# Kernel optimization log

Measured on AMD Instinct MI355X. Metric: run time of the kernel, lower is better.

Reference implementation:

```python
import jax, jax.numpy as jnp
import numpy as np

B, S, D, H_FF, E, NH, K = 8, 1024, 128, 512, 4, 8, 2


def setup_inputs() -> dict:
    key = jax.random.key(0)
    ks = jax.random.split(key, 8)
    g = lambda k, shape, s=0.02: jax.random.normal(k, shape, dtype=jnp.float32) * s
    return {
        "x": jax.random.normal(ks[0], (B, S, D), dtype=jnp.float32),
        "Wqkv": g(ks[1], (D, 3 * D)),
        "bqkv": jnp.zeros((3 * D,), jnp.float32),
        "Wo": g(ks[2], (D, D)),
        "bo": jnp.zeros((D,), jnp.float32),
        "n1_w": jnp.ones((D,), jnp.float32),
        "n1_b": jnp.zeros((D,), jnp.float32),
        "n2_w": jnp.ones((D,), jnp.float32),
        "n2_b": jnp.zeros((D,), jnp.float32),
        "w_gate": g(ks[3], (D, E)),
        "W1": g(ks[4], (E, D, H_FF)),
        "b1": jnp.zeros((E, H_FF), jnp.float32),
        "W2": g(ks[5], (E, H_FF, D)),
        "b2": jnp.zeros((E, D), jnp.float32),
        "num_heads": NH,
        "topk": K,
    }


def _instance_norm(x, w, b, eps=1e-5):
    # InstanceNorm1d applied over the sequence axis, per (batch, channel), affine per channel
    mu = x.mean(axis=1, keepdims=True)
    var = x.var(axis=1, keepdims=True)  # biased variance, as in torch InstanceNorm
    return (x - mu) * jax.lax.rsqrt(var + eps) * w + b


def _cv_sq(v, eps=1e-10):
    return v.var(ddof=1) / (v.mean() ** 2 + eps)


def _forward(x, Wqkv, bqkv, Wo, bo, n1_w, n1_b, n2_w, n2_b, w_gate, W1, b1, W2, b2, num_heads, topk):
    B_, S_, D_ = x.shape
    hd = D_ // num_heads
    # --- MHA ---
    qkv = x @ Wqkv + bqkv  # [B,S,3D]
    q, k, v = jnp.split(qkv, 3, axis=-1)
    rs = lambda t: t.reshape(B_, S_, num_heads, hd).transpose(0, 2, 1, 3)  # [B,H,S,hd]
    q, k, v = rs(q), rs(k), rs(v)
    scores = jnp.einsum('bhqd,bhkd->bhqk', q, k) / jnp.sqrt(jnp.float32(hd))
    attn = jax.nn.softmax(scores, axis=-1)
    o = jnp.einsum('bhqk,bhkd->bhqd', attn, v).transpose(0, 2, 1, 3).reshape(B_, S_, D_)
    h = _instance_norm(o @ Wo + bo + x, n1_w, n1_b)
    # --- MoE feedforward: node-level top-k gating (eval mode: no gating noise) ---
    flat = h.reshape(-1, D_)                      # [N, D], N = B*S tokens
    logits = flat @ w_gate                        # [N, E]
    top_logits, top_idx = jax.lax.top_k(logits, topk)
    top_gates = jax.nn.softmax(top_logits, axis=-1)
    N = flat.shape[0]
    gates = jnp.zeros_like(logits).at[jnp.arange(N)[:, None], top_idx].set(top_gates)
    hid = jax.nn.relu(jnp.einsum('nd,edh->neh', flat, W1) + b1)   # [N,E,H]
    eo = jnp.einsum('neh,ehd->ned', hid, W2) + b2                 # [N,E,D]
    y = jnp.einsum('ne,ned->nd', gates, eo).reshape(B_, S_, D_)
    importance = gates.sum(axis=0)
    load = (gates > 0).astype(jnp.float32).sum(axis=0)
    moe_loss = _cv_sq(importance) + _cv_sq(load)
    out = _instance_norm(y + h, n2_w, n2_b)
    return out, moe_loss


def reference(x, Wqkv, bqkv, Wo, bo, n1_w, n1_b, n2_w, n2_b, w_gate, W1, b1, W2, b2, num_heads, topk):
    out, _moe_loss = _forward(x, Wqkv, bqkv, Wo, bo, n1_w, n1_b, n2_w, n2_b,
                              w_gate, W1, b1, W2, b2, num_heads, topk)
    return out
```

## Files before the change

kernel.cpp:

```cpp
#include <hip/hip_runtime.h>
#include <hip/hip_bf16.h>

#define B_   8
#define S_   1024
#define D_   128
#define NH_  8
#define HD_  16
#define E_   4
#define HFF_ 512
#define NTOK (B_*S_)

typedef unsigned short ushort_t;
typedef __attribute__((ext_vector_type(8))) short bf16x8;
typedef __attribute__((ext_vector_type(4))) float f32x4;
typedef __attribute__((ext_vector_type(4))) _Float16 f16x4;
typedef __attribute__((ext_vector_type(8))) _Float16 f16x8v;

static __device__ __forceinline__ ushort_t f2bf(float f) {
    union { float f; unsigned u; } v; v.f = f;
    unsigned r = v.u + 0x7FFF + ((v.u >> 16) & 1);
    return (ushort_t)(r >> 16);
}
static __device__ __forceinline__ float bf2f(ushort_t u) {
    union { unsigned u; float f; } v; v.u = ((unsigned)u) << 16;
    return v.f;
}

__global__ __launch_bounds__(256)
void prep(const float* __restrict__ x, const float* __restrict__ Wqkv,
          const float* __restrict__ Wo, const float* __restrict__ W1,
          const float* __restrict__ W2,
          ushort_t* __restrict__ xb, ushort_t* __restrict__ Wqkv_t,
          ushort_t* __restrict__ Wo_t, ushort_t* __restrict__ W1t,
          ushort_t* __restrict__ W2t)
{
    const int seg = blockIdx.y;
    const int i = blockIdx.x * 256 + threadIdx.x;
    if (seg == 0) {
        float4 v = ((const float4*)x)[i];
        ushort4 u; u.x = f2bf(v.x); u.y = f2bf(v.y); u.z = f2bf(v.z); u.w = f2bf(v.w);
        ((ushort4*)xb)[i] = u;
    } else if (seg == 1) {
        if (i < D_ * 3 * D_) {
            int r = i / (3 * D_), c = i % (3 * D_);
            Wqkv_t[c * D_ + r] = f2bf(Wqkv[i]);
        }
    } else if (seg == 2) {
        if (i < D_ * D_) {
            int r = i >> 7, c = i & 127;
            Wo_t[c * D_ + r] = f2bf(Wo[i]);
        }
    } else if (seg == 3) {
        int e = i >> 16, rem = i & 65535, r = rem >> 9, c = rem & 511;
        W1t[e * 65536 + c * 128 + r] = f2bf(W1[i]);
    } else {
        int e = i >> 16, rem = i & 65535, k2 = rem >> 7, dd = rem & 127;
        W2t[e * 65536 + dd * 512 + k2] = f2bf(W2[i]);
    }
}

__global__ __launch_bounds__(256)
void gemm_qkv(const ushort_t* __restrict__ A, const ushort_t* __restrict__ Bt,
              const float* __restrict__ bias,
              _Float16* __restrict__ pq, _Float16* __restrict__ pk,
              _Float16* __restrict__ pv)
{
    __shared__ __align__(16) ushort_t As[4][128][8];
    __shared__ __align__(16) ushort_t Bs[4][128][8];
    const int bm = blockIdx.x * 128;
    const int bn = blockIdx.y * 128;
    const int part = blockIdx.y;
    const int tid = threadIdx.x;
    const int l = tid & 63, wv = tid >> 6;
    const int lc = l & 15, lg = l >> 4;
    const int wr = wv >> 1, wc = wv & 1;
    const int K = D_;

    f32x4 acc[4][4] = {};

    const int srow = tid & 127, sch = tid >> 7;
    const ushort_t* ap = A + (size_t)(bm + srow) * K + sch * 8;
    const ushort_t* bp = Bt + (size_t)(bn + srow) * K + sch * 8;

    for (int k0 = 0; k0 < K; k0 += 32) {
        *(bf16x8*)As[sch][srow]     = *(const bf16x8*)(ap + k0);
        *(bf16x8*)As[sch + 2][srow] = *(const bf16x8*)(ap + k0 + 16);
        *(bf16x8*)Bs[sch][srow]     = *(const bf16x8*)(bp + k0);
        *(bf16x8*)Bs[sch + 2][srow] = *(const bf16x8*)(bp + k0 + 16);
        __syncthreads();
        bf16x8 af[4], bfr[4];
        #pragma unroll
        for (int f = 0; f < 4; f++) {
            af[f]  = *(const bf16x8*)As[lg][wr * 64 + f * 16 + lc];
            bfr[f] = *(const bf16x8*)Bs[lg][wc * 64 + f * 16 + lc];
        }
        #pragma unroll
        for (int fm = 0; fm < 4; fm++)
            #pragma unroll
            for (int fn = 0; fn < 4; fn++)
                acc[fm][fn] = __builtin_amdgcn_mfma_f32_16x16x32_bf16(
                    af[fm], bfr[fn], acc[fm][fn], 0, 0, 0);
        __syncthreads();
    }

    #pragma unroll
    for (int fm = 0; fm < 4; fm++) {
        #pragma unroll
        for (int fn = 0; fn < 4; fn++) {
            const int col = bn + wc * 64 + fn * 16 + lc;
            const int hh = (col >> 4) & 7, dd = col & 15;
            const int row0 = bm + wr * 64 + fm * 16 + lg * 4;
            const int b = row0 >> 10, s0 = row0 & 1023;
            const size_t bh = (size_t)(b * NH_ + hh);
            const float bcol = bias[col];
            if (part == 2) {
                f16x4 vv;
                #pragma unroll
                for (int rr = 0; rr < 4; rr++)
                    vv[rr] = (_Float16)(acc[fm][fn][rr] + bcol);
                *(f16x4*)&pv[(bh << 14) + (dd << 10) + s0] = vv;
            } else {
                const float sc = (part == 0) ? 0.36067376022224085f : 1.f;
                _Float16* dst = (part == 0) ? pq : pk;
                #pragma unroll
                for (int rr = 0; rr < 4; rr++)
                    dst[(bh * 1024 + s0 + rr) * HD_ + dd] =
                        (_Float16)((acc[fm][fn][rr] + bcol) * sc);
            }
        }
    }
}

__global__ __launch_bounds__(256)
void gemm_out(const ushort_t* __restrict__ attno, const ushort_t* __restrict__ Wo_t,
              const float* __restrict__ bo, const float* __restrict__ x,
              float* __restrict__ t, float* __restrict__ pstat)
{
    __shared__ __align__(16) ushort_t As[4][64][8];
    __shared__ __align__(16) ushort_t Bs[4][128][8];
    __shared__ float2 sred[4][128];
    const int tok0 = blockIdx.x * 64;
    const int tid = threadIdx.x;
    const int l = tid & 63, wv = tid >> 6;
    const int lc = l & 15, lg = l >> 4;

    f32x4 acc[8] = {};

    const int arow = tid & 63, akc = tid >> 6;
    const int bn = tid & 127, bj = tid >> 7;
    const ushort_t* ap = attno + (size_t)(tok0 + arow) * D_ + akc * 8;
    const ushort_t* bp = Wo_t + (size_t)bn * D_ + bj * 16;

    for (int k0 = 0; k0 < 128; k0 += 32) {
        *(bf16x8*)As[akc][arow]     = *(const bf16x8*)(ap + k0);
        *(bf16x8*)Bs[bj * 2][bn]     = *(const bf16x8*)(bp + k0);
        *(bf16x8*)Bs[bj * 2 + 1][bn] = *(const bf16x8*)(bp + k0 + 8);
        __syncthreads();
        bf16x8 af = *(const bf16x8*)As[lg][wv * 16 + lc];
        #pragma unroll
        for (int fn = 0; fn < 8; fn++) {
            bf16x8 bf = *(const bf16x8*)Bs[lg][fn * 16 + lc];
            acc[fn] = __builtin_amdgcn_mfma_f32_16x16x32_bf16(af, bf, acc[fn], 0, 0, 0);
        }
        __syncthreads();
    }

    const int bb = tok0 >> 10, c16 = (tok0 >> 6) & 15;
    #pragma unroll
    for (int fn = 0; fn < 8; fn++) {
        const int col = fn * 16 + lc;
        float s = 0.f, q = 0.f;
        #pragma unroll
        for (int rr = 0; rr < 4; rr++) {
            const int row = wv * 16 + lg * 4 + rr;
            const size_t off = (size_t)(tok0 + row) * D_ + col;
            float v = acc[fn][rr] + bo[col] + x[off];
            t[off] = v;
            s += v; q += v * v;
        }
        s += __shfl_xor(s, 16); q += __shfl_xor(q, 16);
        s += __shfl_xor(s, 32); q += __shfl_xor(q, 32);
        if (l < 16) sred[wv][col] = make_float2(s, q);
    }
    __syncthreads();
    if (tid < 128) {
        float2 a0 = sred[0][tid], a1 = sred[1][tid], a2 = sred[2][tid], a3 = sred[3][tid];
        ((float2*)pstat)[(bb * 16 + c16) * D_ + tid] =
            make_float2(a0.x + a1.x + a2.x + a3.x, a0.y + a1.y + a2.y + a3.y);
    }
}

__global__ __launch_bounds__(256)
void moe_fused(const ushort_t* __restrict__ hb, const ushort_t* __restrict__ W1t,
               const ushort_t* __restrict__ W2t, const float* __restrict__ b1,
               const float* __restrict__ b2, const float* __restrict__ gates,
               ushort_t* __restrict__ ypartb)
{
    __shared__ __align__(16) ushort_t As[16][64][8];
    __shared__ __align__(16) ushort_t HS[16][64][8];
    const int tok0 = blockIdx.x * 64, e = blockIdx.y;
    const int tid = threadIdx.x;
    const int l = tid & 63, wv = tid >> 6;
    const int lc = l & 15, lg = l >> 4;

    {
        const int row = tid & 63, part = tid >> 6;
        const ushort_t* src = hb + (size_t)(tok0 + row) * D_ + part * 32;
        #pragma unroll
        for (int j = 0; j < 4; j++)
            *(bf16x8*)As[part * 4 + j][row] = *(const bf16x8*)(src + j * 8);
    }
    __syncthreads();

    const ushort_t* W1e = W1t + (size_t)e * HFF_ * D_;
    const ushort_t* W2e = W2t + (size_t)e * D_ * HFF_;
    const int col0 = wv * 32 + lc;

    f32x4 acc2[4][2] = {};

    #pragma unroll 1
    for (int c = 0; c < 4; c++) {
        bf16x8 w1f[4][2], w2f[4][2];
        #pragma unroll
        for (int ks = 0; ks < 4; ks++)
            #pragma unroll
            for (int fn = 0; fn < 2; fn++) {
                w1f[ks][fn] = *(const bf16x8*)&W1e[(size_t)(c * 128 + col0 + fn * 16) * D_ + ks * 32 + lg * 8];
                w2f[ks][fn] = *(const bf16x8*)&W2e[(size_t)(col0 + fn * 16) * HFF_ + c * 128 + ks * 32 + lg * 8];
            }
        f32x4 acc1[4][2] = {};
        #pragma unroll
        for (int ks = 0; ks < 4; ks++) {
            bf16x8 af[4];
            #pragma unroll
            for (int f = 0; f < 4; f++) af[f] = *(const bf16x8*)As[ks * 4 + lg][f * 16 + lc];
            #pragma unroll
            for (int fm = 0; fm < 4; fm++)
                #pragma unroll
                for (int fn = 0; fn < 2; fn++)
                    acc1[fm][fn] = __builtin_amdgcn_mfma_f32_16x16x32_bf16(
                        af[fm], w1f[ks][fn], acc1[fm][fn], 0, 0, 0);
        }
        __syncthreads();
        #pragma unroll
        for (int fm = 0; fm < 4; fm++)
            #pragma unroll
            for (int fn = 0; fn < 2; fn++)
                #pragma unroll
                for (int rr = 0; rr < 4; rr++) {
                    const int row = fm * 16 + lg * 4 + rr;
                    const int col = wv * 32 + fn * 16 + lc;
                    float v = fmaxf(acc1[fm][fn][rr] + b1[e * HFF_ + c * 128 + col], 0.f);
                    HS[col >> 3][row][col & 7] = f2bf(v);
                }
        __syncthreads();
        #pragma unroll
        for (int ks2 = 0; ks2 < 4; ks2++) {
            bf16x8 af[4];
            #pragma unroll
            for (int f = 0; f < 4; f++) af[f] = *(const bf16x8*)HS[ks2 * 4 + lg][f * 16 + lc];
            #pragma unroll
            for (int fm = 0; fm < 4; fm++)
                #pragma unroll
                for (int fn = 0; fn < 2; fn++)
                    acc2[fm][fn] = __builtin_amdgcn_mfma_f32_16x16x32_bf16(
                        af[fm], w2f[ks2][fn], acc2[fm][fn], 0, 0, 0);
        }
    }

    #pragma unroll
    for (int fm = 0; fm < 4; fm++)
        #pragma unroll
        for (int rr = 0; rr < 4; rr++) {
            const int row = fm * 16 + lg * 4 + rr;
            const float g = gates[(size_t)(tok0 + row) * E_ + e];
            #pragma unroll
            for (int fn = 0; fn < 2; fn++) {
                const int d = wv * 32 + fn * 16 + lc;
                ypartb[((size_t)e * NTOK + tok0 + row) * D_ + d] =
                    f2bf(g * (acc2[fm][fn][rr] + b2[e * D_ + d]));
            }
        }
}

#define KT_STR 20
#define VT_STR 136

__global__ __launch_bounds__(256)
void attn_mfma(const _Float16* __restrict__ Qb, const _Float16* __restrict__ Kb,
               const _Float16* __restrict__ Vt, ushort_t* __restrict__ attno)
{
    __shared__ __align__(16) _Float16 KT[2][128 * KT_STR];
    __shared__ __align__(16) _Float16 VTs[2][16 * VT_STR];
    const int bh = blockIdx.x;
    const int tid = threadIdx.x;
    const int wv = tid >> 6;
    const int l  = tid & 63;
    const int r = l & 15, g = l >> 4;
    const int g4 = g * 4;
    const int q0 = blockIdx.y * 128 + wv * 32;

    const _Float16* qp = Qb + ((size_t)bh << 14);
    const _Float16* kp = Kb + ((size_t)bh << 14);
    const _Float16* vp = Vt + ((size_t)bh << 14);

    f16x4 qf0 = *(const f16x4*)&qp[(q0 + r) * HD_ + g4];
    f16x4 qf1 = *(const f16x4*)&qp[(q0 + 16 + r) * HD_ + g4];

    const int krow = tid >> 1, khalf = tid & 1;
    const int kofs = krow * KT_STR + khalf * 8;
    const _Float16* kg = kp + krow * HD_ + khalf * 8;
    const int vrow = tid >> 4, vsc = tid & 15;
    const int vofs = vrow * VT_STR + vsc * 8;
    const _Float16* vg = vp + vrow * 1024 + vsc * 8;

    const int kbase = r * KT_STR + g4;
    const int vbase = r * VT_STR + g4;

    f32x4 o0 = {}, o1 = {};
    float lp0 = 0.f, lp1 = 0.f;

    {
        f16x8v kr = *(const f16x8v*)kg;
        f16x8v vr = *(const f16x8v*)vg;
        *(f16x4*)&KT[0][kofs]     = __builtin_shufflevector(kr, kr, 0, 1, 2, 3);
        *(f16x4*)&KT[0][kofs + 4] = __builtin_shufflevector(kr, kr, 4, 5, 6, 7);
        *(f16x8v*)&VTs[0][vofs]   = vr;
    }
    __syncthreads();

    int cur = 0;
    #pragma unroll 1
    for (int t = 0; t < 8; t++) {
        f16x8v kr, vr;
        if (t < 7) {
            kr = *(const f16x8v*)(kg + (t + 1) * 2048);
            vr = *(const f16x8v*)(vg + (t + 1) * 128);
        }
        const _Float16* KTc = KT[cur];
        const _Float16* VTc = VTs[cur];
        #pragma unroll
        for (int kt = 0; kt < 8; kt++) {
            f16x4 kf = *(const f16x4*)&KTc[kbase + kt * (16 * KT_STR)];
            f16x4 vf = *(const f16x4*)&VTc[vbase + kt * 16];
            f32x4 z = {};
            f32x4 s0 = __builtin_amdgcn_mfma_f32_16x16x16f16(kf, qf0, z, 0, 0, 0);
            f32x4 s1 = __builtin_amdgcn_mfma_f32_16x16x16f16(kf, qf1, z, 0, 0, 0);
            float p0 = exp2f(s0[0]), p1 = exp2f(s0[1]), p2 = exp2f(s0[2]), p3 = exp2f(s0[3]);
            float p4 = exp2f(s1[0]), p5 = exp2f(s1[1]), p6 = exp2f(s1[2]), p7 = exp2f(s1[3]);
            lp0 += (p0 + p1) + (p2 + p3);
            lp1 += (p4 + p5) + (p6 + p7);
            f16x4 pf0, pf1;
            pf0[0] = (_Float16)p0; pf0[1] = (_Float16)p1;
            pf0[2] = (_Float16)p2; pf0[3] = (_Float16)p3;
            pf1[0] = (_Float16)p4; pf1[1] = (_Float16)p5;
            pf1[2] = (_Float16)p6; pf1[3] = (_Float16)p7;
            o0 = __builtin_amdgcn_mfma_f32_16x16x16f16(vf, pf0, o0, 0, 0, 0);
            o1 = __builtin_amdgcn_mfma_f32_16x16x16f16(vf, pf1, o1, 0, 0, 0);
        }
        if (t < 7) {
            *(f16x4*)&KT[cur ^ 1][kofs]     = __builtin_shufflevector(kr, kr, 0, 1, 2, 3);
            *(f16x4*)&KT[cur ^ 1][kofs + 4] = __builtin_shufflevector(kr, kr, 4, 5, 6, 7);
            *(f16x8v*)&VTs[cur ^ 1][vofs]   = vr;
        }
        __syncthreads();
        cur ^= 1;
    }

    lp0 += __shfl_xor(lp0, 16); lp0 += __shfl_xor(lp0, 32);
    lp1 += __shfl_xor(lp1, 16); lp1 += __shfl_xor(lp1, 32);
    const float inv0 = 1.f / lp0, inv1 = 1.f / lp1;

    const int b = bh >> 3, h = bh & 7;
    ushort4 out0, out1;
    out0.x = f2bf(o0[0] * inv0); out0.y = f2bf(o0[1] * inv0);
    out0.z = f2bf(o0[2] * inv0); out0.w = f2bf(o0[3] * inv0);
    out1.x = f2bf(o1[0] * inv1); out1.y = f2bf(o1[1] * inv1);
    out1.z = f2bf(o1[2] * inv1); out1.w = f2bf(o1[3] * inv1);
    *(ushort4*)&attno[((size_t)(b * S_ + q0 + r)) * D_ + h * HD_ + g4] = out0;
    *(ushort4*)&attno[((size_t)(b * S_ + q0 + 16 + r)) * D_ + h * HD_ + g4] = out1;
}

__global__ __launch_bounds__(128)
void moe_reduce_stats(const ushort_t* __restrict__ ypartb, const ushort_t* __restrict__ hb,
                      ushort_t* __restrict__ yhb, float* __restrict__ part)
{
    const int bb = blockIdx.x, chunk = blockIdx.y, d = threadIdx.x;
    float sum = 0.f, sq = 0.f;
    for (int s = 0; s < 32; s++) {
        const size_t off = ((size_t)bb * 1024 + chunk * 32 + s) * D_ + d;
        float v = bf2f(hb[off])
                + bf2f(ypartb[off])
                + bf2f(ypartb[(size_t)1 * NTOK * D_ + off])
                + bf2f(ypartb[(size_t)2 * NTOK * D_ + off])
                + bf2f(ypartb[(size_t)3 * NTOK * D_ + off]);
        yhb[off] = f2bf(v);
        sum += v; sq += v * v;
    }
    ((float2*)part)[(bb * 32 + chunk) * D_ + d] = make_float2(sum, sq);
}

__global__ __launch_bounds__(256)
void in_stats_combine(const float* __restrict__ part, float* __restrict__ stats,
                      int nchunk)
{
    int bd = blockIdx.x * 256 + threadIdx.x;
    if (bd >= B_ * D_) return;
    int bb = bd >> 7, d = bd & 127;
    float sum = 0.f, sq = 0.f;
    const float2* pp = (const float2*)part;
    for (int c = 0; c < nchunk; c++) {
        float2 v = pp[(bb * nchunk + c) * D_ + d];
        sum += v.x; sq += v.y;
    }
    const float invS = 1.f / (float)S_;
    float mu = sum * invS;
    float var = sq * invS - mu * mu;
    ((float2*)stats)[bd] = make_float2(mu, rsqrtf(var + 1e-5f));
}

template<int DUAL, int INBF>
__global__ __launch_bounds__(256)
void in_apply(const void* __restrict__ a, const float* __restrict__ stats,
              const float* __restrict__ w, const float* __restrict__ bias,
              const float* __restrict__ wg, float* __restrict__ outp,
              ushort_t* __restrict__ outb, float* __restrict__ gates)
{
    size_t i4 = (size_t)blockIdx.x * 256 + threadIdx.x;
    int dq = (int)(i4 & 31);
    int tok = (int)(i4 >> 5);
    int bidx = tok >> 10;
    int d0 = dq * 4;
    float4 v;
    if (INBF) {
        ushort4 u = ((const ushort4*)a)[i4];
        v = make_float4(bf2f(u.x), bf2f(u.y), bf2f(u.z), bf2f(u.w));
    } else {
        v = ((const float4*)a)[i4];
    }
    const float2* st = (const float2*)stats;
    float2 s0 = st[bidx * D_ + d0 + 0];
    float2 s1 = st[bidx * D_ + d0 + 1];
    float2 s2 = st[bidx * D_ + d0 + 2];
    float2 s3 = st[bidx * D_ + d0 + 3];
    float4 r;
    r.x = (v.x - s0.x) * s0.y * w[d0 + 0] + bias[d0 + 0];
    r.y = (v.y - s1.x) * s1.y * w[d0 + 1] + bias[d0 + 1];
    r.z = (v.z - s2.x) * s2.y * w[d0 + 2] + bias[d0 + 2];
    r.w = (v.w - s3.x) * s3.y * w[d0 + 3] + bias[d0 + 3];
    if (!DUAL) {
        ((float4*)outp)[i4] = r;
    } else {
        ushort4 ub; ub.x = f2bf(r.x); ub.y = f2bf(r.y); ub.z = f2bf(r.z); ub.w = f2bf(r.w);
        ((ushort4*)outb)[i4] = ub;
        float rv[4] = {r.x, r.y, r.z, r.w};
        float4 aa = make_float4(0.f, 0.f, 0.f, 0.f);
        #pragma unroll
        for (int j = 0; j < 4; j++) {
            float4 wj = ((const float4*)wg)[d0 + j];
            aa.x += rv[j] * wj.x; aa.y += rv[j] * wj.y;
            aa.z += rv[j] * wj.z; aa.w += rv[j] * wj.w;
        }
        #pragma unroll
        for (int msk = 1; msk <= 16; msk <<= 1) {
            aa.x += __shfl_xor(aa.x, msk);
            aa.y += __shfl_xor(aa.y, msk);
            aa.z += __shfl_xor(aa.z, msk);
            aa.w += __shfl_xor(aa.w, msk);
        }
        if (dq == 0) {
            float lv[4] = {aa.x, aa.y, aa.z, aa.w};
            int i0 = 0; float mm0 = lv[0];
            #pragma unroll
            for (int k = 1; k < 4; k++) if (lv[k] > mm0) { mm0 = lv[k]; i0 = k; }
            int i1 = -1; float mm1 = -1e30f;
            #pragma unroll
            for (int k = 0; k < 4; k++) {
                if (k == i0) continue;
                if (lv[k] > mm1) { mm1 = lv[k]; i1 = k; }
            }
            float te = __expf(mm1 - mm0);
            float g0 = 1.f / (1.f + te);
            float g1 = te * g0;
            float gg[4] = {0.f, 0.f, 0.f, 0.f};
            gg[i0] = g0; gg[i1] = g1;
            *(float4*)&gates[(size_t)tok * E_] = make_float4(gg[0], gg[1], gg[2], gg[3]);
        }
    }
}

extern "C" void kernel_launch(void* const* d_in, const int* in_sizes, int n_in,
                              void* d_out, int out_size, void* d_ws, size_t ws_size,
                              hipStream_t stream)
{
    const float* x    = (const float*)d_in[0];
    const float* Wqkv = (const float*)d_in[1];
    const float* bqkv = (const float*)d_in[2];
    const float* Wo   = (const float*)d_in[3];
    const float* bo   = (const float*)d_in[4];
    const float* n1w  = (const float*)d_in[5];
    const float* n1b  = (const float*)d_in[6];
    const float* n2w  = (const float*)d_in[7];
    const float* n2b  = (const float*)d_in[8];
    const float* wg   = (const float*)d_in[9];
    const float* W1   = (const float*)d_in[10];
    const float* b1   = (const float*)d_in[11];
    const float* W2   = (const float*)d_in[12];
    const float* b2   = (const float*)d_in[13];

    char* ws = (char*)d_ws;
    _Float16* Qb     = (_Float16*)(ws);
    _Float16* Kb     = (_Float16*)(ws + (2u << 20));
    _Float16* Vt     = (_Float16*)(ws + (4u << 20));
    ushort_t* attno  = (ushort_t*)(ws + (6u << 20));
    float*    t      = (float*)(ws + (8u << 20));
    ushort_t* hb     = (ushort_t*)(ws + (12u << 20));
    ushort_t* ypartb = (ushort_t*)(ws + (14u << 20));
    ushort_t* yhb    = (ushort_t*)(ws + (22u << 20));
    ushort_t* xb     = (ushort_t*)(ws + (24u << 20));
    char*     wbase  = ws + (26u << 20);
    ushort_t* Wqkv_t = (ushort_t*)(wbase);
    ushort_t* Wo_t   = (ushort_t*)(wbase + (128u << 10));
    ushort_t* W1t    = (ushort_t*)(wbase + (192u << 10));
    ushort_t* W2t    = (ushort_t*)(wbase + (704u << 10));
    float*    gates  = (float*)(wbase + (1216u << 10));
    float*    pstat  = (float*)(wbase + (1344u << 10));
    float*    stats  = (float*)(wbase + (1600u << 10));

    dim3 blk(256);

    prep<<<dim3(1024, 5), blk, 0, stream>>>(x, Wqkv, Wo, W1, W2,
                                            xb, Wqkv_t, Wo_t, W1t, W2t);
    gemm_qkv<<<dim3(64, 3), blk, 0, stream>>>(xb, Wqkv_t, bqkv, Qb, Kb, Vt);
    attn_mfma<<<dim3(64, 8), blk, 0, stream>>>(Qb, Kb, Vt, attno);
    gemm_out<<<dim3(128), blk, 0, stream>>>(attno, Wo_t, bo, x, t, pstat);
    in_stats_combine<<<dim3(4), blk, 0, stream>>>(pstat, stats, 16);
    in_apply<1, 0><<<dim3(1024), blk, 0, stream>>>(t, stats, n1w, n1b, wg,
                                                   nullptr, hb, gates);
    moe_fused<<<dim3(128, 4), blk, 0, stream>>>(hb, W1t, W2t, b1, b2, gates, ypartb);
    moe_reduce_stats<<<dim3(B_, 32), dim3(128), 0, stream>>>(ypartb, hb, yhb, pstat);
    in_stats_combine<<<dim3(4), blk, 0, stream>>>(pstat, stats, 32);
    in_apply<0, 1><<<dim3(1024), blk, 0, stream>>>(yhb, stats, n2w, n2b, nullptr,
                                                   (float*)d_out, nullptr, nullptr);
}
```

Baseline: 106.8 us.

## Route MoE tokens to only their top-2 experts via per-expert token lists

The gating step now builds a per-expert token list with atomic counters and records each token's two chosen experts. The expert kernel gathers only routed tokens and exits early for empty tiles, and the reduce reads only the two active expert outputs instead of all four. This roughly halves the expert GEMM work and the partial-output reads. In exchange it adds a memset, global atomics, gathered row loads, and a nondeterministic token order within each expert list.

After: 225.7 us. 111% more time.

```diff
diff --git a/kernel.cpp b/kernel.cpp
--- a/kernel.cpp
+++ b/kernel.cpp
@@ -194,18 +194,26 @@
 void moe_fused(const ushort_t* __restrict__ hb, const ushort_t* __restrict__ W1t,
                const ushort_t* __restrict__ W2t, const float* __restrict__ b1,
                const float* __restrict__ b2, const float* __restrict__ gates,
+               const int* __restrict__ list, const int* __restrict__ cnt,
                ushort_t* __restrict__ ypartb)
 {
+    const int e = blockIdx.y;
+    const int nt = cnt[e];
+    const int tok0 = blockIdx.x * 64;
+    if (tok0 >= nt) return;
+
     __shared__ __align__(16) ushort_t As[16][64][8];
     __shared__ __align__(16) ushort_t HS[16][64][8];
-    const int tok0 = blockIdx.x * 64, e = blockIdx.y;
+    __shared__ int stok[64];
     const int tid = threadIdx.x;
     const int l = tid & 63, wv = tid >> 6;
     const int lc = l & 15, lg = l >> 4;
 
     {
         const int row = tid & 63, part = tid >> 6;
-        const ushort_t* src = hb + (size_t)(tok0 + row) * D_ + part * 32;
+        const int tok = (tok0 + row < nt) ? list[e * NTOK + tok0 + row] : 0;
+        if (part == 0) stok[row] = tok;
+        const ushort_t* src = hb + (size_t)tok * D_ + part * 32;
         #pragma unroll
         for (int j = 0; j < 4; j++)
             *(bf16x8*)As[part * 4 + j][row] = *(const bf16x8*)(src + j * 8);
@@ -273,12 +281,15 @@
         #pragma unroll
         for (int rr = 0; rr < 4; rr++) {
             const int row = fm * 16 + lg * 4 + rr;
-            const float g = gates[(size_t)(tok0 + row) * E_ + e];
-            #pragma unroll
-            for (int fn = 0; fn < 2; fn++) {
-                const int d = wv * 32 + fn * 16 + lc;
-                ypartb[((size_t)e * NTOK + tok0 + row) * D_ + d] =
-                    f2bf(g * (acc2[fm][fn][rr] + b2[e * D_ + d]));
+            if (tok0 + row < nt) {
+                const int tok = stok[row];
+                const float g = gates[(size_t)tok * E_ + e];
+                #pragma unroll
+                for (int fn = 0; fn < 2; fn++) {
+                    const int d = wv * 32 + fn * 16 + lc;
+                    ypartb[((size_t)e * NTOK + tok) * D_ + d] =
+                        f2bf(g * (acc2[fm][fn][rr] + b2[e * D_ + d]));
+                }
             }
         }
 }
@@ -383,17 +394,19 @@
 
 __global__ __launch_bounds__(128)
 void moe_reduce_stats(const ushort_t* __restrict__ ypartb, const ushort_t* __restrict__ hb,
+                      const int* __restrict__ epair,
                       ushort_t* __restrict__ yhb, float* __restrict__ part)
 {
     const int bb = blockIdx.x, chunk = blockIdx.y, d = threadIdx.x;
     float sum = 0.f, sq = 0.f;
     for (int s = 0; s < 32; s++) {
-        const size_t off = ((size_t)bb * 1024 + chunk * 32 + s) * D_ + d;
+        const int tok = bb * 1024 + chunk * 32 + s;
+        const int ep = epair[tok];
+        const int e0 = ep & 255, e1 = ep >> 8;
+        const size_t off = (size_t)tok * D_ + d;
         float v = bf2f(hb[off])
-                + bf2f(ypartb[off])
-                + bf2f(ypartb[(size_t)1 * NTOK * D_ + off])
-                + bf2f(ypartb[(size_t)2 * NTOK * D_ + off])
-                + bf2f(ypartb[(size_t)3 * NTOK * D_ + off]);
+                + bf2f(ypartb[(size_t)e0 * NTOK * D_ + off])
+                + bf2f(ypartb[(size_t)e1 * NTOK * D_ + off]);
         yhb[off] = f2bf(v);
         sum += v; sq += v * v;
     }
@@ -424,7 +437,9 @@
 void in_apply(const void* __restrict__ a, const float* __restrict__ stats,
               const float* __restrict__ w, const float* __restrict__ bias,
               const float* __restrict__ wg, float* __restrict__ outp,
-              ushort_t* __restrict__ outb, float* __restrict__ gates)
+              ushort_t* __restrict__ outb, float* __restrict__ gates,
+              int* __restrict__ list, int* __restrict__ cnt,
+              int* __restrict__ epair)
 {
     size_t i4 = (size_t)blockIdx.x * 256 + threadIdx.x;
     int dq = (int)(i4 & 31);
@@ -485,6 +500,11 @@
             float gg[4] = {0.f, 0.f, 0.f, 0.f};
             gg[i0] = g0; gg[i1] = g1;
             *(float4*)&gates[(size_t)tok * E_] = make_float4(gg[0], gg[1], gg[2], gg[3]);
+            epair[tok] = i0 | (i1 << 8);
+            int p0 = atomicAdd(&cnt[i0], 1);
+            list[i0 * NTOK + p0] = tok;
+            int p1 = atomicAdd(&cnt[i1], 1);
+            list[i1 * NTOK + p1] = tok;
         }
     }
 }
@@ -526,6 +546,9 @@
     float*    gates  = (float*)(wbase + (1216u << 10));
     float*    pstat  = (float*)(wbase + (1344u << 10));
     float*    stats  = (float*)(wbase + (1600u << 10));
+    int*      list   = (int*)(wbase + (1664u << 10));
+    int*      epair  = (int*)(wbase + (1792u << 10));
+    int*      cnt    = (int*)(wbase + (1824u << 10));
 
     dim3 blk(256);
 
@@ -535,11 +558,16 @@
     attn_mfma<<<dim3(64, 8), blk, 0, stream>>>(Qb, Kb, Vt, attno);
     gemm_out<<<dim3(128), blk, 0, stream>>>(attno, Wo_t, bo, x, t, pstat);
     in_stats_combine<<<dim3(4), blk, 0, stream>>>(pstat, stats, 16);
+    hipMemsetAsync(cnt, 0, 4 * sizeof(int), stream);
     in_apply<1, 0><<<dim3(1024), blk, 0, stream>>>(t, stats, n1w, n1b, wg,
-                                                   nullptr, hb, gates);
-    moe_fused<<<dim3(128, 4), blk, 0, stream>>>(hb, W1t, W2t, b1, b2, gates, ypartb);
-    moe_reduce_stats<<<dim3(B_, 32), dim3(128), 0, stream>>>(ypartb, hb, yhb, pstat);
+                                                   nullptr, hb, gates,
+                                                   list, cnt, epair);
+    moe_fused<<<dim3(128, 4), blk, 0, stream>>>(hb, W1t, W2t, b1, b2, gates,
+                                                list, cnt, ypartb);
+    moe_reduce_stats<<<dim3(B_, 32), dim3(128), 0, stream>>>(ypartb, hb, epair,
+                                                             yhb, pstat);
     in_stats_combine<<<dim3(4), blk, 0, stream>>>(pstat, stats, 32);
     in_apply<0, 1><<<dim3(1024), blk, 0, stream>>>(yhb, stats, n2w, n2b, nullptr,
-                                                   (float*)d_out, nullptr, nullptr);
-}
+                                                   (float*)d_out, nullptr, nullptr,
+                                                   nullptr, nullptr, nullptr);
+}
```
